# Optimization experiments

Hardware: AMD Instinct MI355X
Metric: run time of the kernel (lower is better)

The kernel has to match this reference:

```python
import jax, jax.numpy as jnp
import numpy as np

SIZE = 128
DT = 0.01
DX = 1.0
DY = 1.0
NUM_STEPS = 10
EPS = 1e-6
BATCH = 2048


def smooth3(v):
    # replicate-padded 3-tap mean, matching F.conv1d with ones(3)/3 kernel
    vp = jnp.pad(v, (1, 1), mode='edge')
    return (vp[:-2] + vp[1:-1] + vp[2:]) / 3.0


def thomas(a, b, c, d):
    # a, b, c: (N,) shared across all rows; d: (M, N) batched RHS.
    # Forward elimination coefficients depend only on a,b,c -> scalar scan.
    denom0 = b[0] + EPS
    cs0 = c[0] / denom0

    def fwd_c(c_prev, abc):
        ai, bi, ci = abc
        dn = bi - ai * c_prev + EPS
        cs = ci / dn
        return cs, (cs, dn)

    _, (cs_r, dn_r) = jax.lax.scan(fwd_c, cs0, (a[1:], b[1:], c[1:]))
    c_star = jnp.concatenate([cs0[None], cs_r])          # (N,)

    dT = d.T                                             # (N, M)
    ds0 = dT[0] / denom0

    def fwd_d(d_prev, inp):
        ai, dn, di = inp
        ds = (di - ai * d_prev) / dn
        return ds, ds

    _, ds_r = jax.lax.scan(fwd_d, ds0, (a[1:], dn_r, dT[1:]))
    d_star = jnp.concatenate([ds0[None], ds_r])          # (N, M)

    xN = d_star[-1]

    def bwd(x_next, inp):
        csi, dsi = inp
        xi = dsi - csi * x_next
        return xi, xi

    _, x_r = jax.lax.scan(bwd, xN, (c_star[:-1], d_star[:-1]), reverse=True)
    return jnp.concatenate([x_r, xN[None]]).T            # (M, N)


def diffuse(d2, vec, dt, dh):
    # d2: (M, N) rows to solve; vec: (N,) diffusion coefficient along the solve axis
    coeff = smooth3(vec) * dt / dh ** 2
    a = -coeff
    c = -coeff
    b = 1.0 + 2.0 * coeff
    b = b.at[0].set(1.0 + coeff[0])
    b = b.at[-1].set(1.0 + coeff[-1])
    return thomas(a, b, c, d2)


def _coef(base, lin, quad, t):
    return jnp.clip(base + lin * t + quad * t * t, EPS, None)


def _forward(u, abx, atx, aqx, bby, bty, bqy):
    B, _, H, W = u.shape
    u = u[:, 0]                                          # (B, H, W)
    t = 0.0
    for _ in range(NUM_STEPS):
        # x half-step
        ax = _coef(abx, atx, aqx, t)
        u = diffuse(u.reshape(B * H, W), ax, DT / 2, DX).reshape(B, H, W)
        t += DT / 2
        # y full step (solve along H)
        by = _coef(bby, bty, bqy, t)
        ut = u.transpose(0, 2, 1).reshape(B * W, H)
        u = diffuse(ut, by, DT, DY).reshape(B, W, H).transpose(0, 2, 1)
        t += DT / 2
        # x half-step
        ax = _coef(abx, atx, aqx, t)
        u = diffuse(u.reshape(B * H, W), ax, DT / 2, DX).reshape(B, H, W)
    return u[:, None]                                    # (B, 1, H, W)


def setup_inputs() -> dict:
    key = jax.random.key(0)
    ks = jax.random.split(key, 9)
    u = jax.random.normal(ks[0], (BATCH, 1, SIZE, SIZE), dtype=jnp.float32)
    two = jnp.full((SIZE,), 2.0, dtype=jnp.float32)
    sc = 0.01
    return {
        'u': u,
        'alpha_base_x': two, 'alpha_base_y': two,
        'beta_base_x': two, 'beta_base_y': two,
        'alpha_time_coeff_x': sc * jax.random.normal(ks[1], (SIZE,), jnp.float32),
        'alpha_time_coeff_y': sc * jax.random.normal(ks[2], (SIZE,), jnp.float32),
        'beta_time_coeff_x': sc * jax.random.normal(ks[3], (SIZE,), jnp.float32),
        'beta_time_coeff_y': sc * jax.random.normal(ks[4], (SIZE,), jnp.float32),
        'alpha_time_quad_x': sc * jax.random.normal(ks[5], (SIZE,), jnp.float32),
        'alpha_time_quad_y': sc * jax.random.normal(ks[6], (SIZE,), jnp.float32),
        'beta_time_quad_x': sc * jax.random.normal(ks[7], (SIZE,), jnp.float32),
        'beta_time_quad_y': sc * jax.random.normal(ks[8], (SIZE,), jnp.float32),
    }


def reference(u, alpha_base_x, alpha_base_y, beta_base_x, beta_base_y,
              alpha_time_coeff_x, alpha_time_coeff_y, beta_time_coeff_x, beta_time_coeff_y,
              alpha_time_quad_x, alpha_time_quad_y, beta_time_quad_x, beta_time_quad_y):
    # Note: forward only uses alpha_*_x (x-sweeps) and beta_*_y (y-sweeps),
    # matching the original module's expand_vector_to_matrix usage.
    return _forward(u, alpha_base_x, alpha_time_coeff_x, alpha_time_quad_x,
                    beta_base_y, beta_time_coeff_y, beta_time_quad_y)
```

## Files before the change

### kernel.cpp

```cpp
#include <hip/hip_runtime.h>


#define EPSF 1e-6f
#define STR 132

__device__ float g_FG[30 * 256];

__global__ void factor_kernel(const float* __restrict__ abx,
                              const float* __restrict__ atx,
                              const float* __restrict__ aqx,
                              const float* __restrict__ bby,
                              const float* __restrict__ bty,
                              const float* __restrict__ bqy) {
  const int s = blockIdx.x;
  const int i = threadIdx.x;
  const int step = s / 3, phase = s - 3 * step;
  const float t  = 0.005f * (float)(2 * step + phase);
  const float dt = (phase == 1) ? 0.01f : 0.005f;
  const float* vb = (phase == 1) ? bby : abx;
  const float* vl = (phase == 1) ? bty : atx;
  const float* vq = (phase == 1) ? bqy : aqx;

  __shared__ float vv[128];
  __shared__ float cf[128];

  float v = vb[i] + vl[i] * t + vq[i] * t * t;
  v = fmaxf(v, EPSF);
  vv[i] = v;
  __syncthreads();
  float lft = vv[(i == 0)   ? 0   : (i - 1)];
  float rgt = vv[(i == 127) ? 127 : (i + 1)];
  cf[i] = (lft + v + rgt) * (1.0f / 3.0f) * dt;
  __syncthreads();

  if (i == 0) {
    float* Fo = g_FG + s * 256;
    float* Go = Fo + 128;
    float c0 = cf[0];
    float denom = 1.0f + c0 + EPSF;
    float f = 1.0f / denom;
    float g = c0 * f;
    Fo[0] = f; Go[0] = g;
    float cs = -g;
    for (int k = 1; k < 128; k++) {
      float ck = cf[k];
      float b  = (k == 127) ? (1.0f + ck) : (1.0f + 2.0f * ck);
      float dn = b + ck * cs + EPSF;
      float fk = 1.0f / dn;
      float gk = ck * fk;
      Fo[k] = fk; Go[k] = gk;
      cs = -gk;
    }
  }
}

__device__ __forceinline__ void solve_line(float (&r)[128],
                                           const float* __restrict__ Fs,
                                           const float* __restrict__ Gs) {
  r[0] *= Fs[0];
  #pragma unroll
  for (int i = 1; i < 128; i++) r[i] = fmaf(Gs[i], r[i - 1], r[i] * Fs[i]);
  #pragma unroll
  for (int i = 126; i >= 0; i--) r[i] = fmaf(Gs[i], r[i + 1], r[i]);
}

template <int REPS>
__device__ __forceinline__ void x_session(float* __restrict__ sm, int tid,
                                          const float* __restrict__ FG) {
  float r[128];
  #pragma unroll
  for (int q = 0; q < 32; q++) {
    float4 t = *(const float4*)&sm[tid * STR + 4 * q];
    r[4 * q + 0] = t.x; r[4 * q + 1] = t.y;
    r[4 * q + 2] = t.z; r[4 * q + 3] = t.w;
  }
  #pragma unroll
  for (int rep = 0; rep < REPS; rep++) solve_line(r, FG, FG + 128);
  #pragma unroll
  for (int q = 0; q < 32; q++) {
    float4 t;
    t.x = r[4 * q + 0]; t.y = r[4 * q + 1];
    t.z = r[4 * q + 2]; t.w = r[4 * q + 3];
    *(float4*)&sm[tid * STR + 4 * q] = t;
  }
}

__device__ __forceinline__ void y_session(float* __restrict__ sm, int tid,
                                          const float* __restrict__ FG) {
  float r[128];
  #pragma unroll
  for (int h = 0; h < 128; h++) r[h] = sm[h * STR + tid];
  solve_line(r, FG, FG + 128);
  #pragma unroll
  for (int h = 0; h < 128; h++) sm[h * STR + tid] = r[h];
}

__global__ __launch_bounds__(128, 1) void diffusion_kernel(
    const float* __restrict__ uin,
    float* __restrict__ uout) {
  extern __shared__ float sm[];
  const int tid = threadIdx.x;
  const long long ibase = (long long)blockIdx.x << 14;

  #pragma unroll
  for (int k = 0; k < 16384; k += 512) {
    int idx = k + tid * 4;
    int h = idx >> 7, w = idx & 127;
    *(float4*)&sm[h * STR + w] = *(const float4*)(uin + ibase + idx);
  }
  __syncthreads();

  x_session<1>(sm, tid, g_FG);
  __syncthreads();
  #pragma unroll 1
  for (int k = 0; k < 10; k++) {
    y_session(sm, tid, g_FG + (3 * k + 1) * 256);
    __syncthreads();
    if (k < 9) x_session<2>(sm, tid, g_FG + (3 * k + 2) * 256);
    else       x_session<1>(sm, tid, g_FG + (3 * k + 2) * 256);
    __syncthreads();
  }

  #pragma unroll
  for (int k = 0; k < 16384; k += 512) {
    int idx = k + tid * 4;
    int h = idx >> 7, w = idx & 127;
    *(float4*)(uout + ibase + idx) = *(const float4*)&sm[h * STR + w];
  }
}

extern "C" void kernel_launch(void* const* d_in, const int* in_sizes, int n_in,
                              void* d_out, int out_size, void* d_ws, size_t ws_size,
                              hipStream_t stream) {
  const float* u   = (const float*)d_in[0];
  const float* abx = (const float*)d_in[1];
  const float* bby = (const float*)d_in[4];
  const float* atx = (const float*)d_in[5];
  const float* bty = (const float*)d_in[8];
  const float* aqx = (const float*)d_in[9];
  const float* bqy = (const float*)d_in[12];
  float* out = (float*)d_out;

  factor_kernel<<<30, 128, 0, stream>>>(abx, atx, aqx, bby, bty, bqy);
  diffusion_kernel<<<2048, 128, STR * 128 * sizeof(float), stream>>>(u, out);
}
```

Baseline: 509.0 us.

## Keep tile in registers and transpose through half-size LDS buffer between sweeps

The full 128x128 tile no longer lives in shared memory. Each thread now keeps its line in registers and loads and stores global memory directly by rows. Between x and y sweeps, a two-phase transpose goes through a 128x65 LDS buffer, which halves LDS use. Launch bounds are raised to two blocks per CU to improve occupancy. In exchange, each transpose adds extra barriers and a 64-float temporary, which adds register pressure and risks spills at the higher occupancy target.

```diff
diff --git a/kernel.cpp b/kernel.cpp
--- a/kernel.cpp
+++ b/kernel.cpp
@@ -2,7 +2,7 @@
 
 
 #define EPSF 1e-6f
-#define STR 132
+#define TSTR 65
 
 __device__ float g_FG[30 * 256];
 
@@ -64,68 +64,90 @@
   for (int i = 126; i >= 0; i--) r[i] = fmaf(Gs[i], r[i + 1], r[i]);
 }
 
-template <int REPS>
-__device__ __forceinline__ void x_session(float* __restrict__ sm, int tid,
-                                          const float* __restrict__ FG) {
-  float r[128];
+__device__ __forceinline__ void transpose_lds(float (&r)[128],
+                                              float* __restrict__ buf,
+                                              int tid) {
+  const int lane = tid & 63;
+  __syncthreads();
   #pragma unroll
-  for (int q = 0; q < 32; q++) {
-    float4 t = *(const float4*)&sm[tid * STR + 4 * q];
-    r[4 * q + 0] = t.x; r[4 * q + 1] = t.y;
-    r[4 * q + 2] = t.z; r[4 * q + 3] = t.w;
+  for (int q = 0; q < 16; q++) {
+    float4 t;
+    t.x = r[4*q+0]; t.y = r[4*q+1]; t.z = r[4*q+2]; t.w = r[4*q+3];
+    *(float4*)&buf[tid * TSTR + 4*q] = t;
   }
-  #pragma unroll
-  for (int rep = 0; rep < REPS; rep++) solve_line(r, FG, FG + 128);
-  #pragma unroll
-  for (int q = 0; q < 32; q++) {
-    float4 t;
-    t.x = r[4 * q + 0]; t.y = r[4 * q + 1];
-    t.z = r[4 * q + 2]; t.w = r[4 * q + 3];
-    *(float4*)&sm[tid * STR + 4 * q] = t;
+  __syncthreads();
+  float tmp[64];
+  if (tid < 64) {
+    #pragma unroll
+    for (int j = 0; j < 64; j++) tmp[j] = r[64 + j];
+    #pragma unroll
+    for (int h = 0; h < 128; h++) r[h] = buf[h * TSTR + lane];
+  }
+  __syncthreads();
+  if (tid < 64) {
+    #pragma unroll
+    for (int q = 0; q < 16; q++) {
+      float4 t;
+      t.x = tmp[4*q+0]; t.y = tmp[4*q+1]; t.z = tmp[4*q+2]; t.w = tmp[4*q+3];
+      *(float4*)&buf[tid * TSTR + 4*q] = t;
+    }
+  } else {
+    #pragma unroll
+    for (int q = 0; q < 16; q++) {
+      float4 t;
+      t.x = r[64+4*q+0]; t.y = r[64+4*q+1]; t.z = r[64+4*q+2]; t.w = r[64+4*q+3];
+      *(float4*)&buf[tid * TSTR + 4*q] = t;
+    }
+  }
+  __syncthreads();
+  if (tid >= 64) {
+    #pragma unroll
+    for (int h = 0; h < 128; h++) r[h] = buf[h * TSTR + lane];
   }
 }
 
-__device__ __forceinline__ void y_session(float* __restrict__ sm, int tid,
-                                          const float* __restrict__ FG) {
-  float r[128];
-  #pragma unroll
-  for (int h = 0; h < 128; h++) r[h] = sm[h * STR + tid];
-  solve_line(r, FG, FG + 128);
-  #pragma unroll
-  for (int h = 0; h < 128; h++) sm[h * STR + tid] = r[h];
-}
-
-__global__ __launch_bounds__(128, 1) void diffusion_kernel(
+__global__ __launch_bounds__(128, 2) void diffusion_kernel(
     const float* __restrict__ uin,
     float* __restrict__ uout) {
-  extern __shared__ float sm[];
+  __shared__ float buf[128 * TSTR];
   const int tid = threadIdx.x;
   const long long ibase = (long long)blockIdx.x << 14;
 
-  #pragma unroll
-  for (int k = 0; k < 16384; k += 512) {
-    int idx = k + tid * 4;
-    int h = idx >> 7, w = idx & 127;
-    *(float4*)&sm[h * STR + w] = *(const float4*)(uin + ibase + idx);
+  float r[128];
+
+  {
+    const float* gin = uin + ibase + tid * 128;
+    #pragma unroll
+    for (int q = 0; q < 32; q++) {
+      float4 t = *(const float4*)(gin + 4*q);
+      r[4*q+0] = t.x; r[4*q+1] = t.y; r[4*q+2] = t.z; r[4*q+3] = t.w;
+    }
   }
-  __syncthreads();
 
-  x_session<1>(sm, tid, g_FG);
-  __syncthreads();
+  solve_line(r, g_FG, g_FG + 128);
+  transpose_lds(r, buf, tid);
+
   #pragma unroll 1
   for (int k = 0; k < 10; k++) {
-    y_session(sm, tid, g_FG + (3 * k + 1) * 256);
-    __syncthreads();
-    if (k < 9) x_session<2>(sm, tid, g_FG + (3 * k + 2) * 256);
-    else       x_session<1>(sm, tid, g_FG + (3 * k + 2) * 256);
-    __syncthreads();
+    const float* FGy = g_FG + (3 * k + 1) * 256;
+    solve_line(r, FGy, FGy + 128);
+    transpose_lds(r, buf, tid);
+    const float* FGx = g_FG + (3 * k + 2) * 256;
+    solve_line(r, FGx, FGx + 128);
+    if (k < 9) {
+      solve_line(r, FGx, FGx + 128);
+      transpose_lds(r, buf, tid);
+    }
   }
 
-  #pragma unroll
-  for (int k = 0; k < 16384; k += 512) {
-    int idx = k + tid * 4;
-    int h = idx >> 7, w = idx & 127;
-    *(float4*)(uout + ibase + idx) = *(const float4*)&sm[h * STR + w];
+  {
+    float* gout = uout + ibase + tid * 128;
+    #pragma unroll
+    for (int q = 0; q < 32; q++) {
+      float4 t;
+      t.x = r[4*q+0]; t.y = r[4*q+1]; t.z = r[4*q+2]; t.w = r[4*q+3];
+      *(float4*)(gout + 4*q) = t;
+    }
   }
 }
 
@@ -142,5 +164,5 @@
   float* out = (float*)d_out;
 
   factor_kernel<<<30, 128, 0, stream>>>(abx, atx, aqx, bby, bty, bqy);
-  diffusion_kernel<<<2048, 128, STR * 128 * sizeof(float), stream>>>(u, out);
+  diffusion_kernel<<<2048, 128, 0, stream>>>(u, out);
 }
```

Result: slower. 617.5 us (+21.3%).
